# Performance work log

Hardware: AMD Instinct MI355X
Metric: run time of the kernel (lower is better)

## Reference

```python
import jax, jax.numpy as jnp
import numpy as np

H_Q = 32      # num_attention_heads
H_KV = 8      # num_key_value_heads
D = 128       # head_dim
WIN = 127     # left window size (flash window_size=(127,-1))
BLK = 128


def setup_inputs() -> dict:
    key = jax.random.key(0)
    kq, kk, kv = jax.random.split(key, 3)
    B, S = 2, 4096
    Q = jax.random.normal(kq, (B, S, H_Q * D), dtype=jnp.float32)
    K = jax.random.normal(kk, (B, S, H_KV * D), dtype=jnp.float32)
    V = jax.random.normal(kv, (B, S, H_KV * D), dtype=jnp.float32)
    return {"Q": Q, "K": K, "V": V}


def _banded_mask(nblk):
    # query row r in block n has global index n*BLK + r
    # key col c in window indexes global key (n-1)*BLK + c,  c in [0, 2*BLK)
    r = jnp.arange(BLK)[:, None]
    c = jnp.arange(2 * BLK)[None, :]
    base = (c <= r + BLK) & (c >= r + BLK - WIN)          # [BLK, 2BLK]
    n = jnp.arange(nblk)[:, None, None]
    valid_pad = (n > 0) | (c[None] >= BLK)                # block 0 has zero-padded left keys
    return base[None] & valid_pad                          # [nblk, BLK, 2BLK]


def reference(Q, K, V):
    B, S, _ = Q.shape
    nblk = S // BLK
    g = H_Q // H_KV
    scale = 1.0 / np.sqrt(D)

    # [B, Hkv, g, nblk, BLK, D]
    q = Q.reshape(B, S, H_Q, D).transpose(0, 2, 1, 3).reshape(B, H_KV, g, nblk, BLK, D)
    k = K.reshape(B, S, H_KV, D).transpose(0, 2, 1, 3)   # [B, Hkv, S, D]
    v = V.reshape(B, S, H_KV, D).transpose(0, 2, 1, 3)

    # pad one zero block in front, then build 2-block sliding windows
    pad = jnp.zeros((B, H_KV, BLK, D), dtype=K.dtype)
    kp = jnp.concatenate([pad, k], axis=2).reshape(B, H_KV, nblk + 1, BLK, D)
    vp = jnp.concatenate([pad, v], axis=2).reshape(B, H_KV, nblk + 1, BLK, D)
    kwin = jnp.concatenate([kp[:, :, :-1], kp[:, :, 1:]], axis=3)  # [B,Hkv,nblk,2BLK,D]
    vwin = jnp.concatenate([vp[:, :, :-1], vp[:, :, 1:]], axis=3)

    scores = jnp.einsum('bhgnrd,bhncd->bhgnrc', q, kwin) * scale   # [B,Hkv,g,nblk,BLK,2BLK]
    mask = _banded_mask(nblk)                                      # [nblk,BLK,2BLK]
    scores = jnp.where(mask[None, None, None], scores, jnp.finfo(scores.dtype).min)
    p = jax.nn.softmax(scores, axis=-1)
    out = jnp.einsum('bhgnrc,bhncd->bhgnrd', p, vwin)              # [B,Hkv,g,nblk,BLK,D]
    out = out.reshape(B, H_Q, S, D).transpose(0, 2, 1, 3).reshape(B, S, H_Q * D)
    return out
```

## Files before the change

kernel.cpp:

```cpp
#include <hip/hip_runtime.h>
#include <stdint.h>

#define S_LEN 4096
#define HQ 32
#define HKV 8
#define DD 128
#define QBLK 128
#define KVROW (HKV * DD)

typedef __attribute__((ext_vector_type(8)))  __bf16 bf16x8;
typedef __attribute__((ext_vector_type(2)))  __bf16 bf16x2;
typedef __attribute__((ext_vector_type(4)))  float  f32x4;
typedef __attribute__((ext_vector_type(2)))  unsigned int u32x2;
typedef __attribute__((ext_vector_type(4)))  unsigned int u32x4;

__device__ __forceinline__ unsigned int pk2(float lo, float hi2) {
  bf16x2 t = {(__bf16)lo, (__bf16)hi2};
  return __builtin_bit_cast(unsigned int, t);
}
__device__ __forceinline__ bf16x8 mk8(unsigned int w0, unsigned int w1,
                                      unsigned int w2, unsigned int w3) {
  u32x4 u = {w0, w1, w2, w3};
  return __builtin_bit_cast(bf16x8, u);
}

#define SWZV(d) ((((d) & 15) ^ ((d) >> 4)) << 3)

__global__ __launch_bounds__(1024, 1)
void swa_fwd(const float* __restrict__ Qg, const float* __restrict__ Kg,
             const float* __restrict__ Vg, float* __restrict__ Og) {
  __shared__ __align__(16) unsigned char Kl[65536];
  __shared__ __align__(16) unsigned char Vl[65536];

  const int nwg  = gridDim.x;
  const int bid0 = blockIdx.x;
  const int bid  = (bid0 & 7) * (nwg >> 3) + (bid0 >> 3);

  const int n    = bid & 31;
  const int hkv  = (bid >> 5) & 7;
  const int b    = bid >> 8;
  const int tid  = threadIdx.x;
  const int lane = tid & 63;
  const int wv   = tid >> 6;
  const int g    = lane >> 4;
  const int l15  = lane & 15;

  #pragma unroll
  for (int i = 0; i < 8; ++i) {
    const int e  = i * 1024 + tid;
    const int c  = e >> 5;
    const int dc = e & 31;
    const int tk = (n - 1) * QBLK + c;
    f32x4 xk = {0.f, 0.f, 0.f, 0.f};
    f32x4 xv = {0.f, 0.f, 0.f, 0.f};
    if (tk >= 0) {
      const size_t base = (size_t)(b * S_LEN + tk) * KVROW + hkv * DD + dc * 4;
      xk = *(const f32x4*)(Kg + base);
      xv = *(const f32x4*)(Vg + base);
    }
    u32x2 kw = { pk2(xk[0], xk[1]), pk2(xk[2], xk[3]) };
    *(u32x2*)(&Kl[c * 256 + ((dc * 8) ^ ((c & 15) << 4))]) = kw;
    #pragma unroll
    for (int j = 0; j < 4; ++j) {
      const int d = dc * 4 + j;
      *(unsigned short*)(&Vl[d * 512 + ((c * 2) ^ SWZV(d))]) =
          __builtin_bit_cast(unsigned short, (__bf16)xv[j]);
    }
  }
  __syncthreads();

  const float SC = 0.08838834764831845f * 1.44269504088896340f;

  #pragma unroll 1
  for (int uu = 0; uu < 2; ++uu) {
    const int uid   = wv * 2 + uu;
    const int h     = hkv * 4 + (uid >> 3);
    const int chunk = uid & 7;
    const int qs    = chunk * 16;

    const float* qp = Qg + (size_t)(b * S_LEN + n * QBLK + qs + l15) * (HQ * DD)
                      + h * DD + g * 8;
    bf16x8 qf[4];
    #pragma unroll
    for (int dc = 0; dc < 4; ++dc) {
      f32x4 a  = *(const f32x4*)(qp + dc * 32);
      f32x4 c4 = *(const f32x4*)(qp + dc * 32 + 4);
      qf[dc] = mk8(pk2(a[0], a[1]), pk2(a[2], a[3]),
                   pk2(c4[0], c4[1]), pk2(c4[2], c4[3]));
    }

    f32x4 o[8];
    #pragma unroll
    for (int dt = 0; dt < 8; ++dt) o[dt] = (f32x4){0.f, 0.f, 0.f, 0.f};
    float ls = 0.f;

    #pragma unroll
    for (int pp = 0; pp < 5; ++pp) {
      const int tt0 = 2 * pp, tt1 = 2 * pp + 1;
      if (n == 0 && chunk + tt1 < 8) continue;

      unsigned int w0 = 0, w1 = 0, w2 = 0, w3 = 0;

      if (!(n == 0 && chunk + tt0 < 8)) {
        const int c = (chunk + tt0) * 16 + l15;
        f32x4 acc = {0.f, 0.f, 0.f, 0.f};
        __builtin_amdgcn_s_setprio(1);
        #pragma unroll
        for (int dc = 0; dc < 4; ++dc) {
          const bf16x8 kf = *(const bf16x8*)(
              &Kl[c * 256 + ((dc * 64 + g * 16) ^ ((c & 15) << 4))]);
          acc = __builtin_amdgcn_mfma_f32_16x16x32_bf16(kf, qf[dc], acc, 0, 0, 0);
        }
        __builtin_amdgcn_s_setprio(0);
        float p[4];
        #pragma unroll
        for (int r = 0; r < 4; ++r) {
          const int g4r = g * 4 + r;
          const float e = __builtin_amdgcn_exp2f(acc[r] * SC);
          bool valid = true;
          if (pp == 0) valid = (g4r > l15);
          if (pp == 4) valid = (g4r <= l15);
          p[r] = valid ? e : 0.f;
          ls += p[r];
        }
        w0 = pk2(p[0], p[1]);
        w1 = pk2(p[2], p[3]);
      }

      if (pp < 4 && !(n == 0 && chunk + tt1 < 8)) {
        const int c = (chunk + tt1) * 16 + l15;
        f32x4 acc = {0.f, 0.f, 0.f, 0.f};
        __builtin_amdgcn_s_setprio(1);
        #pragma unroll
        for (int dc = 0; dc < 4; ++dc) {
          const bf16x8 kf = *(const bf16x8*)(
              &Kl[c * 256 + ((dc * 64 + g * 16) ^ ((c & 15) << 4))]);
          acc = __builtin_amdgcn_mfma_f32_16x16x32_bf16(kf, qf[dc], acc, 0, 0, 0);
        }
        __builtin_amdgcn_s_setprio(0);
        float p0 = __builtin_amdgcn_exp2f(acc[0] * SC);
        float p1 = __builtin_amdgcn_exp2f(acc[1] * SC);
        float p2 = __builtin_amdgcn_exp2f(acc[2] * SC);
        float p3 = __builtin_amdgcn_exp2f(acc[3] * SC);
        ls += p0 + p1 + p2 + p3;
        w2 = pk2(p0, p1);
        w3 = pk2(p2, p3);
      }

      const bf16x8 pf = mk8(w0, w1, w2, w3);
      const int ck0 = ((chunk + tt0) * 16 + g * 4) * 2;
      const int ck1 = (pp < 4) ? ((chunk + tt1) * 16 + g * 4) * 2 : ck0;
      __builtin_amdgcn_s_setprio(1);
      #pragma unroll
      for (int dt = 0; dt < 8; ++dt) {
        const int d  = dt * 16 + l15;
        const int rb = d * 512;
        const int sz = SWZV(d);
        const u32x2 a0 = *(const u32x2*)(&Vl[rb + (ck0 ^ sz)]);
        const u32x2 a1 = *(const u32x2*)(&Vl[rb + (ck1 ^ sz)]);
        const bf16x8 vf = mk8(a0[0], a0[1], a1[0], a1[1]);
        o[dt] = __builtin_amdgcn_mfma_f32_16x16x32_bf16(vf, pf, o[dt], 0, 0, 0);
      }
      __builtin_amdgcn_s_setprio(0);
    }

    ls += __shfl_xor(ls, 16);
    ls += __shfl_xor(ls, 32);
    const float inv = 1.0f / ls;

    float* op = Og + (size_t)(b * S_LEN + n * QBLK + qs + l15) * (HQ * DD)
                + h * DD + g * 4;
    #pragma unroll
    for (int dt = 0; dt < 8; ++dt) {
      f32x4 v = o[dt];
      v[0] *= inv; v[1] *= inv; v[2] *= inv; v[3] *= inv;
      *(f32x4*)(op + dt * 16) = v;
    }
  }
}

extern "C" void kernel_launch(void* const* d_in, const int* in_sizes, int n_in,
                              void* d_out, int out_size, void* d_ws, size_t ws_size,
                              hipStream_t stream) {
  const float* Q = (const float*)d_in[0];
  const float* K = (const float*)d_in[1];
  const float* V = (const float*)d_in[2];
  float* O = (float*)d_out;
  const int B = in_sizes[0] / (S_LEN * HQ * DD);
  const int nblocks = B * HKV * (S_LEN / QBLK);
  swa_fwd<<<dim3(nblocks), dim3(1024), 0, stream>>>(Q, K, V, O);
}
```

Baseline: 94.08 us.

## Split each query block across four smaller workgroups with reduced K/V staging

Each 128-row query block is now divided into four workgroups of 512 threads, each covering 32 query rows. Each workgroup stages only the 160 keys its band needs (40 KB each for K and V instead of 64 KB), and each wave handles a single 16-row chunk instead of looping over two. The V swizzle is changed to fit the new 320-byte row stride. This gives more, smaller workgroups with several resident per CU, improving occupancy and overlap of loads with compute. In exchange, K/V rows that neighbouring sub-blocks share are loaded and converted more than once.

New measurement: 85.68 us. 8.9% less time.

```diff
diff --git a/kernel.cpp b/kernel.cpp
--- a/kernel.cpp
+++ b/kernel.cpp
@@ -24,33 +24,35 @@
   return __builtin_bit_cast(bf16x8, u);
 }
 
-#define SWZV(d) ((((d) & 15) ^ ((d) >> 4)) << 3)
+#define SWZV(d) ((((d) & 7) ^ (((d) >> 4) & 7)) << 3)
 
-__global__ __launch_bounds__(1024, 1)
+__global__ __launch_bounds__(512, 4)
 void swa_fwd(const float* __restrict__ Qg, const float* __restrict__ Kg,
              const float* __restrict__ Vg, float* __restrict__ Og) {
-  __shared__ __align__(16) unsigned char Kl[65536];
-  __shared__ __align__(16) unsigned char Vl[65536];
+  __shared__ __align__(16) unsigned char Kl[40960];
+  __shared__ __align__(16) unsigned char Vl[40960];
 
   const int nwg  = gridDim.x;
   const int bid0 = blockIdx.x;
   const int bid  = (bid0 & 7) * (nwg >> 3) + (bid0 >> 3);
 
-  const int n    = bid & 31;
-  const int hkv  = (bid >> 5) & 7;
-  const int b    = bid >> 8;
+  const int j    = bid & 3;
+  const int n    = (bid >> 2) & 31;
+  const int hkv  = (bid >> 7) & 7;
+  const int b    = bid >> 10;
   const int tid  = threadIdx.x;
   const int lane = tid & 63;
   const int wv   = tid >> 6;
   const int g    = lane >> 4;
   const int l15  = lane & 15;
 
+  const int kbase = (n - 1) * QBLK + 32 * j;
   #pragma unroll
-  for (int i = 0; i < 8; ++i) {
-    const int e  = i * 1024 + tid;
+  for (int i = 0; i < 10; ++i) {
+    const int e  = i * 512 + tid;
     const int c  = e >> 5;
     const int dc = e & 31;
-    const int tk = (n - 1) * QBLK + c;
+    const int tk = kbase + c;
     f32x4 xk = {0.f, 0.f, 0.f, 0.f};
     f32x4 xv = {0.f, 0.f, 0.f, 0.f};
     if (tk >= 0) {
@@ -61,121 +63,116 @@
     u32x2 kw = { pk2(xk[0], xk[1]), pk2(xk[2], xk[3]) };
     *(u32x2*)(&Kl[c * 256 + ((dc * 8) ^ ((c & 15) << 4))]) = kw;
     #pragma unroll
-    for (int j = 0; j < 4; ++j) {
-      const int d = dc * 4 + j;
-      *(unsigned short*)(&Vl[d * 512 + ((c * 2) ^ SWZV(d))]) =
-          __builtin_bit_cast(unsigned short, (__bf16)xv[j]);
+    for (int j4 = 0; j4 < 4; ++j4) {
+      const int d = dc * 4 + j4;
+      *(unsigned short*)(&Vl[d * 320 + ((c * 2) ^ SWZV(d))]) =
+          __builtin_bit_cast(unsigned short, (__bf16)xv[j4]);
     }
   }
   __syncthreads();
 
   const float SC = 0.08838834764831845f * 1.44269504088896340f;
 
-  #pragma unroll 1
-  for (int uu = 0; uu < 2; ++uu) {
-    const int uid   = wv * 2 + uu;
-    const int h     = hkv * 4 + (uid >> 3);
-    const int chunk = uid & 7;
-    const int qs    = chunk * 16;
+  const int cc = wv & 1;
+  const int h  = hkv * 4 + (wv >> 1);
+  const int cg = 2 * j + cc;
+  const int qrow = n * QBLK + 32 * j + cc * 16 + l15;
 
-    const float* qp = Qg + (size_t)(b * S_LEN + n * QBLK + qs + l15) * (HQ * DD)
-                      + h * DD + g * 8;
-    bf16x8 qf[4];
-    #pragma unroll
-    for (int dc = 0; dc < 4; ++dc) {
-      f32x4 a  = *(const f32x4*)(qp + dc * 32);
-      f32x4 c4 = *(const f32x4*)(qp + dc * 32 + 4);
-      qf[dc] = mk8(pk2(a[0], a[1]), pk2(a[2], a[3]),
-                   pk2(c4[0], c4[1]), pk2(c4[2], c4[3]));
+  const float* qp = Qg + (size_t)(b * S_LEN + qrow) * (HQ * DD) + h * DD + g * 8;
+  bf16x8 qf[4];
+  #pragma unroll
+  for (int dc = 0; dc < 4; ++dc) {
+    f32x4 a  = *(const f32x4*)(qp + dc * 32);
+    f32x4 c4 = *(const f32x4*)(qp + dc * 32 + 4);
+    qf[dc] = mk8(pk2(a[0], a[1]), pk2(a[2], a[3]),
+                 pk2(c4[0], c4[1]), pk2(c4[2], c4[3]));
+  }
+
+  f32x4 o[8];
+  #pragma unroll
+  for (int dt = 0; dt < 8; ++dt) o[dt] = (f32x4){0.f, 0.f, 0.f, 0.f};
+  float ls = 0.f;
+
+  #pragma unroll
+  for (int pp = 0; pp < 5; ++pp) {
+    const int tt0 = 2 * pp, tt1 = 2 * pp + 1;
+    if (n == 0 && cg + tt1 < 8) continue;
+
+    unsigned int w0 = 0, w1 = 0, w2 = 0, w3 = 0;
+
+    if (!(n == 0 && cg + tt0 < 8)) {
+      const int c = (cc + tt0) * 16 + l15;
+      f32x4 acc = {0.f, 0.f, 0.f, 0.f};
+      __builtin_amdgcn_s_setprio(1);
+      #pragma unroll
+      for (int dc = 0; dc < 4; ++dc) {
+        const bf16x8 kf = *(const bf16x8*)(
+            &Kl[c * 256 + ((dc * 64 + g * 16) ^ ((c & 15) << 4))]);
+        acc = __builtin_amdgcn_mfma_f32_16x16x32_bf16(kf, qf[dc], acc, 0, 0, 0);
+      }
+      __builtin_amdgcn_s_setprio(0);
+      float p[4];
+      #pragma unroll
+      for (int r = 0; r < 4; ++r) {
+        const int g4r = g * 4 + r;
+        const float e = __builtin_amdgcn_exp2f(acc[r] * SC);
+        bool valid = true;
+        if (pp == 0) valid = (g4r > l15);
+        if (pp == 4) valid = (g4r <= l15);
+        p[r] = valid ? e : 0.f;
+        ls += p[r];
+      }
+      w0 = pk2(p[0], p[1]);
+      w1 = pk2(p[2], p[3]);
     }
 
-    f32x4 o[8];
-    #pragma unroll
-    for (int dt = 0; dt < 8; ++dt) o[dt] = (f32x4){0.f, 0.f, 0.f, 0.f};
-    float ls = 0.f;
-
-    #pragma unroll
-    for (int pp = 0; pp < 5; ++pp) {
-      const int tt0 = 2 * pp, tt1 = 2 * pp + 1;
-      if (n == 0 && chunk + tt1 < 8) continue;
-
-      unsigned int w0 = 0, w1 = 0, w2 = 0, w3 = 0;
-
-      if (!(n == 0 && chunk + tt0 < 8)) {
-        const int c = (chunk + tt0) * 16 + l15;
-        f32x4 acc = {0.f, 0.f, 0.f, 0.f};
-        __builtin_amdgcn_s_setprio(1);
-        #pragma unroll
-        for (int dc = 0; dc < 4; ++dc) {
-          const bf16x8 kf = *(const bf16x8*)(
-              &Kl[c * 256 + ((dc * 64 + g * 16) ^ ((c & 15) << 4))]);
-          acc = __builtin_amdgcn_mfma_f32_16x16x32_bf16(kf, qf[dc], acc, 0, 0, 0);
-        }
-        __builtin_amdgcn_s_setprio(0);
-        float p[4];
-        #pragma unroll
-        for (int r = 0; r < 4; ++r) {
-          const int g4r = g * 4 + r;
-          const float e = __builtin_amdgcn_exp2f(acc[r] * SC);
-          bool valid = true;
-          if (pp == 0) valid = (g4r > l15);
-          if (pp == 4) valid = (g4r <= l15);
-          p[r] = valid ? e : 0.f;
-          ls += p[r];
-        }
-        w0 = pk2(p[0], p[1]);
-        w1 = pk2(p[2], p[3]);
-      }
-
-      if (pp < 4 && !(n == 0 && chunk + tt1 < 8)) {
-        const int c = (chunk + tt1) * 16 + l15;
-        f32x4 acc = {0.f, 0.f, 0.f, 0.f};
-        __builtin_amdgcn_s_setprio(1);
-        #pragma unroll
-        for (int dc = 0; dc < 4; ++dc) {
-          const bf16x8 kf = *(const bf16x8*)(
-              &Kl[c * 256 + ((dc * 64 + g * 16) ^ ((c & 15) << 4))]);
-          acc = __builtin_amdgcn_mfma_f32_16x16x32_bf16(kf, qf[dc], acc, 0, 0, 0);
-        }
-        __builtin_amdgcn_s_setprio(0);
-        float p0 = __builtin_amdgcn_exp2f(acc[0] * SC);
-        float p1 = __builtin_amdgcn_exp2f(acc[1] * SC);
-        float p2 = __builtin_amdgcn_exp2f(acc[2] * SC);
-        float p3 = __builtin_amdgcn_exp2f(acc[3] * SC);
-        ls += p0 + p1 + p2 + p3;
-        w2 = pk2(p0, p1);
-        w3 = pk2(p2, p3);
-      }
-
-      const bf16x8 pf = mk8(w0, w1, w2, w3);
-      const int ck0 = ((chunk + tt0) * 16 + g * 4) * 2;
-      const int ck1 = (pp < 4) ? ((chunk + tt1) * 16 + g * 4) * 2 : ck0;
+    if (pp < 4 && !(n == 0 && cg + tt1 < 8)) {
+      const int c = (cc + tt1) * 16 + l15;
+      f32x4 acc = {0.f, 0.f, 0.f, 0.f};
       __builtin_amdgcn_s_setprio(1);
       #pragma unroll
-      for (int dt = 0; dt < 8; ++dt) {
-        const int d  = dt * 16 + l15;
-        const int rb = d * 512;
-        const int sz = SWZV(d);
-        const u32x2 a0 = *(const u32x2*)(&Vl[rb + (ck0 ^ sz)]);
-        const u32x2 a1 = *(const u32x2*)(&Vl[rb + (ck1 ^ sz)]);
-        const bf16x8 vf = mk8(a0[0], a0[1], a1[0], a1[1]);
-        o[dt] = __builtin_amdgcn_mfma_f32_16x16x32_bf16(vf, pf, o[dt], 0, 0, 0);
+      for (int dc = 0; dc < 4; ++dc) {
+        const bf16x8 kf = *(const bf16x8*)(
+            &Kl[c * 256 + ((dc * 64 + g * 16) ^ ((c & 15) << 4))]);
+        acc = __builtin_amdgcn_mfma_f32_16x16x32_bf16(kf, qf[dc], acc, 0, 0, 0);
       }
       __builtin_amdgcn_s_setprio(0);
+      float p0 = __builtin_amdgcn_exp2f(acc[0] * SC);
+      float p1 = __builtin_amdgcn_exp2f(acc[1] * SC);
+      float p2 = __builtin_amdgcn_exp2f(acc[2] * SC);
+      float p3 = __builtin_amdgcn_exp2f(acc[3] * SC);
+      ls += p0 + p1 + p2 + p3;
+      w2 = pk2(p0, p1);
+      w3 = pk2(p2, p3);
     }
 
-    ls += __shfl_xor(ls, 16);
-    ls += __shfl_xor(ls, 32);
-    const float inv = 1.0f / ls;
-
-    float* op = Og + (size_t)(b * S_LEN + n * QBLK + qs + l15) * (HQ * DD)
-                + h * DD + g * 4;
+    const bf16x8 pf = mk8(w0, w1, w2, w3);
+    const int ck0 = ((cc + tt0) * 16 + g * 4) * 2;
+    const int ck1 = (pp < 4) ? ((cc + tt1) * 16 + g * 4) * 2 : ck0;
+    __builtin_amdgcn_s_setprio(1);
     #pragma unroll
     for (int dt = 0; dt < 8; ++dt) {
-      f32x4 v = o[dt];
-      v[0] *= inv; v[1] *= inv; v[2] *= inv; v[3] *= inv;
-      *(f32x4*)(op + dt * 16) = v;
+      const int d  = dt * 16 + l15;
+      const int rb = d * 320;
+      const int sz = SWZV(d);
+      const u32x2 a0 = *(const u32x2*)(&Vl[rb + (ck0 ^ sz)]);
+      const u32x2 a1 = *(const u32x2*)(&Vl[rb + (ck1 ^ sz)]);
+      const bf16x8 vf = mk8(a0[0], a0[1], a1[0], a1[1]);
+      o[dt] = __builtin_amdgcn_mfma_f32_16x16x32_bf16(vf, pf, o[dt], 0, 0, 0);
     }
+    __builtin_amdgcn_s_setprio(0);
+  }
+
+  ls += __shfl_xor(ls, 16);
+  ls += __shfl_xor(ls, 32);
+  const float inv = 1.0f / ls;
+
+  float* op = Og + (size_t)(b * S_LEN + qrow) * (HQ * DD) + h * DD + g * 4;
+  #pragma unroll
+  for (int dt = 0; dt < 8; ++dt) {
+    f32x4 v = o[dt];
+    v[0] *= inv; v[1] *= inv; v[2] *= inv; v[3] *= inv;
+    *(f32x4*)(op + dt * 16) = v;
   }
 }
 
@@ -187,6 +184,6 @@
   const float* V = (const float*)d_in[2];
   float* O = (float*)d_out;
   const int B = in_sizes[0] / (S_LEN * HQ * DD);
-  const int nblocks = B * HKV * (S_LEN / QBLK);
-  swa_fwd<<<dim3(nblocks), dim3(1024), 0, stream>>>(Q, K, V, O);
+  const int nblocks = B * HKV * (S_LEN / QBLK) * 4;
+  swa_fwd<<<dim3(nblocks), dim3(512), 0, stream>>>(Q, K, V, O);
 }
```
